# Performance work log

Measured on AMD Instinct MI355X. Metric: run time of the kernel, lower is better.

## Reference

```python
import jax, jax.numpy as jnp
import numpy as np

DEMO_T = 4
N_HEADS = 4
N_LAYERS = 2
EPS = 1e-5
IN_DIM = 512
FF_DIM = 128
TEMP = float(np.sqrt(IN_DIM))  # temperature=None -> sqrt(in_dim)


def setup_inputs() -> dict:
    key = jax.random.key(0)
    ks = jax.random.split(key, 12)
    B, d, T, H, W = 8, IN_DIM, 36, 7, 12
    s_in = 1.0 / np.sqrt(d)
    s_ff = 1.0 / np.sqrt(FF_DIM)
    f32 = jnp.float32
    return {
        "inputs": jax.random.normal(ks[0], (B, d, T, H, W), f32),
        "demo_wq": jax.random.normal(ks[1], (N_LAYERS, FF_DIM, d), f32) * s_in,
        "demo_wk": jax.random.normal(ks[2], (N_LAYERS, FF_DIM, d), f32) * s_in,
        "demo_wv": jax.random.normal(ks[3], (N_LAYERS, FF_DIM, d), f32) * s_in,
        "demo_wo": jax.random.normal(ks[4], (N_LAYERS, d, FF_DIM), f32) * s_ff,
        "obs_wq": jax.random.normal(ks[5], (N_LAYERS, FF_DIM, d), f32) * s_in,
        "obs_wk": jax.random.normal(ks[6], (N_LAYERS, FF_DIM, d), f32) * s_in,
        "obs_wv": jax.random.normal(ks[7], (N_LAYERS, FF_DIM, d), f32) * s_in,
        "obs_wo": jax.random.normal(ks[8], (N_LAYERS, d, FF_DIM), f32) * s_ff,
        "bn_gamma": jnp.ones((N_LAYERS, d), f32),
        "bn_beta": jnp.zeros((N_LAYERS, d), f32),
    }


def _conv1x1(w, x):
    # 1x1x1 Conv3d, bias=False == per-voxel channel mixing
    return jnp.einsum('od,bdthw->bothw', w, x)


def _forward(inputs, demo_wq, demo_wk, demo_wv, demo_wo,
             obs_wq, obs_wk, obs_wv, obs_wo, bn_gamma, bn_beta):
    B, d, T, H, W = inputs.shape
    HW = H * W
    obs_T = T - DEMO_T
    neg_inf = jnp.asarray(-jnp.inf, inputs.dtype)
    # causal log-mask over demo tokens, block-expanded to spatial positions
    tril = jnp.tril(jnp.ones((DEMO_T, DEMO_T), inputs.dtype))
    mask = jnp.repeat(jnp.repeat(tril, HW, axis=0), HW, axis=1)  # (dTHW, dTHW)
    log_mask = jnp.where(mask > 0, jnp.asarray(0.0, inputs.dtype), neg_inf)

    x = inputs
    for i in range(N_LAYERS):
        demo_in = x[:, :, :DEMO_T]   # [B,d,dT,H,W]
        obs_in = x[:, :, DEMO_T:]    # [B,d,oT,H,W]

        # --- demo self-attention (causal) ---
        def demo_heads(w):
            y = _conv1x1(w, demo_in)                      # [B,ff,dT,H,W]
            return y.reshape(B, N_HEADS, -1, DEMO_T * HW)  # [B,n,ch,dTHW]
        dq, dk, dv = demo_heads(demo_wq[i]), demo_heads(demo_wk[i]), demo_heads(demo_wv[i])
        dkq = jnp.einsum('bnci,bncj->bnij', dk, dq) / TEMP + log_mask
        dattn = jax.nn.softmax(dkq, axis=-1)               # softmax over j (as in source)
        dv_att = jnp.einsum('bncj,bnij->bnci', dv, dattn)  # attended demo values
        # NOTE: the source computes demo_out via demo_Outs + relu-skip but never
        # uses it downstream (dead code); only dv_att/dk feed the obs fusion.

        # --- obs attention, fused with demo keys/attended-values ---
        def obs_heads(w):
            y = _conv1x1(w, obs_in)                        # [B,ff,oT,H,W]
            y = y.reshape(B, N_HEADS, -1, obs_T, HW)
            return jnp.transpose(y, (0, 3, 1, 2, 4))       # [B,oT,n,ch,HW]
        oq, ok, ov = obs_heads(obs_wq[i]), obs_heads(obs_wk[i]), obs_heads(obs_wv[i])
        rep_k = jnp.broadcast_to(dk[:, None], (B, obs_T) + dk.shape[1:])
        rep_v = jnp.broadcast_to(dv_att[:, None], (B, obs_T) + dv_att.shape[1:])
        cat_k = jnp.concatenate([rep_k, ok], axis=-1)      # [B,oT,n,ch,(1+dT)HW]
        cat_v = jnp.concatenate([rep_v, ov], axis=-1)
        okq = jnp.einsum('btnci,btncj->btnij', cat_k, oq) / TEMP  # i=cat len, j=HW
        oattn = jax.nn.softmax(okq, axis=-1)               # softmax over j (source: dim=4)
        ov_att = jnp.einsum('btncj,btnji->btnci', cat_v, oattn)  # [B,oT,n,ch,HW]
        obs_out = _conv1x1(obs_wo[i],
                           jnp.transpose(ov_att, (0, 2, 3, 1, 4)).reshape(B, -1, obs_T, H, W))
        # skip (out_dim == in_dim), dropout=0 -> identity
        obs_res = obs_in + jax.nn.relu(obs_out)

        # shared BatchNorm3d (training-mode batch stats) over concatenated streams
        x = jnp.concatenate([demo_in, obs_res], axis=2)
        mean = x.mean(axis=(0, 2, 3, 4)).reshape(1, -1, 1, 1, 1)
        var = x.var(axis=(0, 2, 3, 4)).reshape(1, -1, 1, 1, 1)
        g = bn_gamma[i].reshape(1, -1, 1, 1, 1)
        b = bn_beta[i].reshape(1, -1, 1, 1, 1)
        x = g * (x - mean) * jax.lax.rsqrt(var + EPS) + b
    return x  # == out_dict['last']


def reference(inputs, demo_wq, demo_wk, demo_wv, demo_wo,
              obs_wq, obs_wk, obs_wv, obs_wo, bn_gamma, bn_beta):
    return _forward(inputs, demo_wq, demo_wk, demo_wv, demo_wo,
                    obs_wq, obs_wk, obs_wv, obs_wo, bn_gamma, bn_beta)
```

## Files before the change

### kernel.cpp

```cpp
#include <hip/hip_runtime.h>

#define B_N 8
#define D_N 512
#define T_N 36
#define HW_N 84
#define THW_N 3024
#define DT_N 4
#define OT_N 32
#define NH_N 4
#define FF_N 128
#define CH_N 32
#define DI_N 336
#define OI_N 2688
#define CAT_N 420
#define INV_TEMP 0.04419417382415922f
#define BN_EPS 1e-5f
#define INV_CNT (1.0f / 24192.0f)

#define SW_DWQ 0
#define SW_DWK 131072
#define SW_DWV 262144
#define SW_OWQ 393216
#define SW_OWK 524288
#define SW_OWV 655360
#define SW_OWO 786432
#define S_DQ   917504
#define S_DK   1261568
#define S_DV   1605632
#define S_DVA  1949696
#define S_OQ   2293760
#define S_OK   5046272
#define S_OV   7798784
#define S_OVA  10551296
#define S_XBF  13303808

typedef short bf16x8 __attribute__((ext_vector_type(8)));
typedef float f32x4 __attribute__((ext_vector_type(4)));

__device__ __forceinline__ short f2bf(float f) {
    unsigned u = __float_as_uint(f);
    u += 0x7fffu + ((u >> 16) & 1u);
    return (short)(u >> 16);
}
__device__ __forceinline__ float bf2f(short s) {
    return __uint_as_float(((unsigned)(unsigned short)s) << 16);
}

__global__ __launch_bounds__(256) void cvt_w_kernel(
    const float* __restrict__ s0, const float* __restrict__ s1,
    const float* __restrict__ s2, const float* __restrict__ s3,
    const float* __restrict__ s4, const float* __restrict__ s5,
    const float* __restrict__ s6, short* __restrict__ dst,
    float* __restrict__ stats)
{
    const int bid = blockIdx.x;
    if (bid == 0) {
        #pragma unroll
        for (int k = 0; k < 8; ++k) stats[threadIdx.x * 8 + k] = 0.f;
    }
    const int a = bid >> 6, blk = bid & 63;
    const float* src;
    switch (a) {
        case 0: src = s0; break; case 1: src = s1; break;
        case 2: src = s2; break; case 3: src = s3; break;
        case 4: src = s4; break; case 5: src = s5; break;
        default: src = s6;
    }
    const int idx = (blk * 256 + (int)threadIdx.x) * 8;
    float4 f0 = *reinterpret_cast<const float4*>(src + idx);
    float4 f1 = *reinterpret_cast<const float4*>(src + idx + 4);
    bf16x8 pk;
    pk[0] = f2bf(f0.x); pk[1] = f2bf(f0.y); pk[2] = f2bf(f0.z); pk[3] = f2bf(f0.w);
    pk[4] = f2bf(f1.x); pk[5] = f2bf(f1.y); pk[6] = f2bf(f1.z); pk[7] = f2bf(f1.w);
    *reinterpret_cast<bf16x8*>(dst + (size_t)a * 131072 + idx) = pk;
}

__global__ __launch_bounds__(256) void xin_kernel(
    const float* __restrict__ in_f, short* __restrict__ xbf,
    float* __restrict__ stats0)
{
    __shared__ short tile[48][65];
    __shared__ float red_s[16][64];
    __shared__ float red_q[16][64];

    const int bid = blockIdx.x;
    const int b = bid / 504, rem = bid % 504, tt = rem >> 3, cblk = rem & 7;
    const int t0 = tt * 48, c0 = cblk * 64;
    const int tid = threadIdx.x;
    const bool is_demo = (tt < 7);

    #pragma unroll
    for (int l0 = 0; l0 < 768; l0 += 256) {
        int l = l0 + tid;
        int cc = l / 12, tg = l % 12;
        size_t addr = ((size_t)b * D_N + c0 + cc) * THW_N + t0 + tg * 4;
        float4 v = *reinterpret_cast<const float4*>(in_f + addr);
        tile[tg * 4 + 0][cc] = f2bf(v.x);
        tile[tg * 4 + 1][cc] = f2bf(v.y);
        tile[tg * 4 + 2][cc] = f2bf(v.z);
        tile[tg * 4 + 3][cc] = f2bf(v.w);
    }
    __syncthreads();
    float psum[4] = {}, psq[4] = {};
    const int cg = tid & 15;
    #pragma unroll
    for (int l0 = 0; l0 < 768; l0 += 256) {
        int l = l0 + tid;
        int tk = l >> 4;
        short4 s4;
        s4.x = tile[tk][cg * 4 + 0];
        s4.y = tile[tk][cg * 4 + 1];
        s4.z = tile[tk][cg * 4 + 2];
        s4.w = tile[tk][cg * 4 + 3];
        *reinterpret_cast<short4*>(
            xbf + ((size_t)b * THW_N + t0 + tk) * 512 + c0 + cg * 4) = s4;
        if (is_demo) {
            float v0 = bf2f(s4.x), v1 = bf2f(s4.y), v2 = bf2f(s4.z), v3 = bf2f(s4.w);
            psum[0] += v0; psum[1] += v1; psum[2] += v2; psum[3] += v3;
            psq[0] += v0 * v0; psq[1] += v1 * v1; psq[2] += v2 * v2; psq[3] += v3 * v3;
        }
    }
    if (!is_demo) return;
    __syncthreads();
    #pragma unroll
    for (int j = 0; j < 4; ++j) {
        red_s[tid >> 4][cg * 4 + j] = psum[j];
        red_q[tid >> 4][cg * 4 + j] = psq[j];
    }
    __syncthreads();
    if (tid < 64) {
        float s = 0.f, q = 0.f;
        #pragma unroll
        for (int r = 0; r < 16; ++r) { s += red_s[r][tid]; q += red_q[r][tid]; }
        atomicAdd(&stats0[c0 + tid], s);
        atomicAdd(&stats0[512 + c0 + tid], q);
    }
}

__global__ __launch_bounds__(256) void proj_mfma_kernel(
    const short* __restrict__ xbf, short* __restrict__ ws, int layer)
{
    __shared__ short As[3][4096];
    __shared__ short Bs[1536];

    const int bid = blockIdx.x;
    const int b = bid / 63, ct = bid - b * 63;
    const bool is_demo = (ct < 7);
    const int woff = layer * 65536;
    const short* W0 = ws + (is_demo ? SW_DWQ : SW_OWQ) + woff;
    const short* W1 = ws + (is_demo ? SW_DWK : SW_OWK) + woff;
    const short* W2 = ws + (is_demo ? SW_DWV : SW_OWV) + woff;
    const int Ltok = is_demo ? DI_N : OI_N;
    const int colL = is_demo ? ct * 48 : (ct - 7) * 48;
    short* Yq = ws + (is_demo ? S_DQ : S_OQ);
    short* Yk = ws + (is_demo ? S_DK : S_OK);
    short* Yv = ws + (is_demo ? S_DV : S_OV);
    const short* Xb = xbf + ((size_t)b * THW_N + (is_demo ? 0 : DI_N) + colL) * 512;

    const int tid = threadIdx.x;
    const int lane = tid & 63, wv = tid >> 6;
    const int l15 = lane & 15, q = lane >> 4;

    f32x4 acc[3][2][3] = {};

    for (int k0 = 0; k0 < D_N; k0 += 32) {
        __syncthreads();
        const short* Wt[3] = {W0, W1, W2};
        #pragma unroll
        for (int wt = 0; wt < 3; ++wt) {
            #pragma unroll
            for (int h = 0; h < 2; ++h) {
                int c = tid + h * 256;
                int kc = c & 3, m = c >> 2;
                bf16x8 pk = *reinterpret_cast<const bf16x8*>(
                    Wt[wt] + (size_t)m * D_N + k0 + kc * 8);
                *reinterpret_cast<bf16x8*>(&As[wt][(kc * 128 + m) * 8]) = pk;
            }
        }
        if (tid < 192) {
            int n = tid % 48, kc = tid / 48;
            bf16x8 pk = *reinterpret_cast<const bf16x8*>(
                Xb + (size_t)n * 512 + k0 + kc * 8);
            *reinterpret_cast<bf16x8*>(&Bs[(kc * 48 + n) * 8]) = pk;
        }
        __syncthreads();

        bf16x8 bfr[3];
        #pragma unroll
        for (int nt = 0; nt < 3; ++nt)
            bfr[nt] = *reinterpret_cast<const bf16x8*>(&Bs[(q * 48 + nt * 16 + l15) * 8]);
        #pragma unroll
        for (int wt = 0; wt < 3; ++wt) {
            #pragma unroll
            for (int mt2 = 0; mt2 < 2; ++mt2) {
                bf16x8 afr = *reinterpret_cast<const bf16x8*>(
                    &As[wt][(q * 128 + wv * 32 + mt2 * 16 + l15) * 8]);
                #pragma unroll
                for (int nt = 0; nt < 3; ++nt)
                    acc[wt][mt2][nt] = __builtin_amdgcn_mfma_f32_16x16x32_bf16(
                        afr, bfr[nt], acc[wt][mt2][nt], 0, 0, 0);
            }
        }
    }

    #pragma unroll
    for (int mt2 = 0; mt2 < 2; ++mt2) {
        int mrow = wv * 32 + mt2 * 16 + q * 4;
        #pragma unroll
        for (int nt = 0; nt < 3; ++nt) {
            int token = colL + nt * 16 + l15;
            f32x4 aq = acc[0][mt2][nt] * INV_TEMP;
            short4 s4;
            s4.x = f2bf(aq[0]); s4.y = f2bf(aq[1]); s4.z = f2bf(aq[2]); s4.w = f2bf(aq[3]);
            *reinterpret_cast<short4*>(Yq + ((size_t)b * Ltok + token) * 128 + mrow) = s4;
            f32x4 ak = acc[1][mt2][nt];
            s4.x = f2bf(ak[0]); s4.y = f2bf(ak[1]); s4.z = f2bf(ak[2]); s4.w = f2bf(ak[3]);
            *reinterpret_cast<short4*>(Yk + ((size_t)b * Ltok + token) * 128 + mrow) = s4;
            #pragma unroll
            for (int r = 0; r < 4; ++r)
                Yv[((size_t)b * FF_N + mrow + r) * Ltok + token] = f2bf(acc[2][mt2][nt][r]);
        }
    }
}

template<int NT>
__device__ __forceinline__ void demo_core(
    const short* __restrict__ dqS, const short* __restrict__ dkS,
    const short* __restrict__ dvS, short* __restrict__ dvaS,
    short* __restrict__ Pt, int b, int n, int ti, int ih)
{
    constexpr int NTP = (NT + 1) & ~1;
    const int tid = threadIdx.x;
    const int lane = tid & 63, w = tid >> 6;
    const int l15 = lane & 15, q = lane >> 4;
    const int jmax = (ti + 1) * 84;

    const int irow = ih * 48 + w * 16 + l15;
    const int tokA = ti * 84 + (irow < 84 ? irow : 83);
    bf16x8 afr = *reinterpret_cast<const bf16x8*>(
        dkS + ((size_t)b * DI_N + tokA) * 128 + n * 32 + q * 8);

    f32x4 s[NT];
    #pragma unroll
    for (int nt = 0; nt < NT; ++nt) {
        bf16x8 bfr = *reinterpret_cast<const bf16x8*>(
            dqS + ((size_t)b * DI_N + nt * 16 + l15) * 128 + n * 32 + q * 8);
        f32x4 z = {};
        s[nt] = __builtin_amdgcn_mfma_f32_16x16x32_bf16(afr, bfr, z, 0, 0, 0);
    }

    const int mstart = jmax - (NT - 1) * 16;
    #pragma unroll
    for (int r = 0; r < 4; ++r) {
        if (l15 >= mstart) s[NT - 1][r] = -3.0e38f;
        float mx = s[0][r];
        #pragma unroll
        for (int nt = 1; nt < NT; ++nt) mx = fmaxf(mx, s[nt][r]);
        #pragma unroll
        for (int o = 1; o < 16; o <<= 1) mx = fmaxf(mx, __shfl_xor(mx, o));
        float sm = 0.f;
        #pragma unroll
        for (int nt = 0; nt < NT; ++nt) {
            float e = __expf(s[nt][r] - mx);
            s[nt][r] = e; sm += e;
        }
        #pragma unroll
        for (int o = 1; o < 16; o <<= 1) sm += __shfl_xor(sm, o);
        float inv = 1.f / sm;
        #pragma unroll
        for (int nt = 0; nt < NT; ++nt) s[nt][r] *= inv;
    }

    #pragma unroll
    for (int nt = 0; nt < NT; ++nt)
        #pragma unroll
        for (int r = 0; r < 4; ++r)
            Pt[(w * 16 + q * 4 + r) * 360 + nt * 16 + l15] = f2bf(s[nt][r]);
    if (NTP != NT) {
        #pragma unroll
        for (int r = 0; r < 4; ++r)
            Pt[(w * 16 + q * 4 + r) * 360 + NT * 16 + l15] = 0;
    }
    __syncthreads();

    f32x4 oacc[2] = {};
    #pragma unroll
    for (int kk = 0; kk < NTP / 2; ++kk) {
        bf16x8 pb = *reinterpret_cast<const bf16x8*>(
            &Pt[(w * 16 + l15) * 360 + kk * 32 + q * 8]);
        #pragma unroll
        for (int ct = 0; ct < 2; ++ct) {
            bf16x8 va = *reinterpret_cast<const bf16x8*>(
                dvS + ((size_t)b * FF_N + n * 32 + ct * 16 + l15) * DI_N + kk * 32 + q * 8);
            oacc[ct] = __builtin_amdgcn_mfma_f32_16x16x32_bf16(va, pb, oacc[ct], 0, 0, 0);
        }
    }

    const int ig = ih * 48 + w * 16 + l15;
    if (ig < 84) {
        #pragma unroll
        for (int ct = 0; ct < 2; ++ct)
            #pragma unroll
            for (int r = 0; r < 4; ++r)
                dvaS[((size_t)b * FF_N + n * 32 + ct * 16 + q * 4 + r) * DI_N + ti * 84 + ig] =
                    f2bf(oacc[ct][r]);
    }
}

__global__ __launch_bounds__(192) void demo_attn_mfma_kernel(const short* __restrict__ ws)
{
    __shared__ short Pt[48 * 360];

    const short* dqS = ws + S_DQ;
    const short* dkS = ws + S_DK;
    const short* dvS = ws + S_DV;
    short* dvaS = const_cast<short*>(ws) + S_DVA;

    const int bid = blockIdx.x;
    const int ih = bid & 1, ti = (bid >> 1) & 3;
    const int n = (bid >> 3) & 3, b = bid >> 5;

    switch (ti) {
        case 0: demo_core<6>(dqS, dkS, dvS, dvaS, Pt, b, n, ti, ih); break;
        case 1: demo_core<11>(dqS, dkS, dvS, dvaS, Pt, b, n, ti, ih); break;
        case 2: demo_core<16>(dqS, dkS, dvS, dvaS, Pt, b, n, ti, ih); break;
        default: demo_core<21>(dqS, dkS, dvS, dvaS, Pt, b, n, ti, ih); break;
    }
}

__global__ __launch_bounds__(256, 4) void obs_attn_mfma_kernel(const short* __restrict__ ws)
{
    __shared__ short Qt[96 * 40];
    __shared__ short Kt[64 * 40];
    __shared__ short Vs[32 * 72];
    __shared__ short Pt[96 * 72];

    const short* dkS = ws + S_DK;
    const short* dvaS = ws + S_DVA;
    const short* oqS = ws + S_OQ;
    const short* okS = ws + S_OK;
    const short* ovS = ws + S_OV;
    short* ovaS = const_cast<short*>(ws) + S_OVA;

    const int bid = blockIdx.x;
    const int b = bid >> 7, rem = bid & 127, t = rem >> 2, n = rem & 3;

    const int tid = threadIdx.x;
    const int lane = tid & 63, wv = tid >> 6;
    const int l15 = lane & 15, q = lane >> 4;

    for (int l = tid; l < 384; l += 256) {
        int i = l >> 2, c0 = (l & 3) * 8;
        bf16x8 pk = {0,0,0,0,0,0,0,0};
        if (i < HW_N)
            pk = *reinterpret_cast<const bf16x8*>(
                oqS + ((size_t)b * OI_N + t * 84 + i) * 128 + n * 32 + c0);
        *reinterpret_cast<bf16x8*>(&Qt[i * 40 + c0]) = pk;
    }

    const int pv_mt = wv & 1;
    const int pv_nb = wv >> 1;
    f32x4 oacc[3] = {};

    for (int jc = 0; jc < 448; jc += 64) {
        __syncthreads();
        {
            int jl = tid >> 2, c0 = (tid & 3) * 8;
            int jg = jc + jl;
            bf16x8 pk = {0,0,0,0,0,0,0,0};
            if (jg < DI_N)
                pk = *reinterpret_cast<const bf16x8*>(
                    dkS + ((size_t)b * DI_N + jg) * 128 + n * 32 + c0);
            else if (jg < CAT_N)
                pk = *reinterpret_cast<const bf16x8*>(
                    okS + ((size_t)b * OI_N + t * 84 + (jg - DI_N)) * 128 + n * 32 + c0);
            *reinterpret_cast<bf16x8*>(&Kt[jl * 40 + c0]) = pk;
        }
        {
            int c = tid >> 3, j0 = (tid & 7) * 8;
            int jg0 = jc + j0;
            const short* dvaRow = dvaS + ((size_t)b * FF_N + n * 32 + c) * DI_N;
            const short* ovRow = ovS + ((size_t)b * FF_N + n * 32 + c) * OI_N + t * 84;
            bf16x8 pk;
            if (jg0 + 8 <= DI_N) {
                pk = *reinterpret_cast<const bf16x8*>(dvaRow + jg0);
            } else if (jg0 >= DI_N && jg0 + 8 <= CAT_N) {
                short4 lo = *reinterpret_cast<const short4*>(ovRow + (jg0 - DI_N));
                short4 hi = *reinterpret_cast<const short4*>(ovRow + (jg0 - DI_N) + 4);
                pk[0]=lo.x; pk[1]=lo.y; pk[2]=lo.z; pk[3]=lo.w;
                pk[4]=hi.x; pk[5]=hi.y; pk[6]=hi.z; pk[7]=hi.w;
            } else {
                #pragma unroll
                for (int p = 0; p < 8; ++p) {
                    int jg = jg0 + p;
                    pk[p] = (jg < DI_N) ? dvaRow[jg]
                          : ((jg < CAT_N) ? ovRow[jg - DI_N] : (short)0);
                }
            }
            *reinterpret_cast<bf16x8*>(&Vs[c * 72 + j0]) = pk;
        }
        __syncthreads();

        f32x4 s[6];
        bf16x8 afr = *reinterpret_cast<const bf16x8*>(&Kt[(wv * 16 + l15) * 40 + q * 8]);
        #pragma unroll
        for (int nt = 0; nt < 6; ++nt) {
            bf16x8 bfr = *reinterpret_cast<const bf16x8*>(&Qt[(nt * 16 + l15) * 40 + q * 8]);
            f32x4 z = {};
            s[nt] = __builtin_amdgcn_mfma_f32_16x16x32_bf16(afr, bfr, z, 0, 0, 0);
        }
        float inv[4];
        #pragma unroll
        for (int r = 0; r < 4; ++r) {
            if (l15 >= 4) s[5][r] = -3.0e38f;
            float m2 = s[0][r];
            #pragma unroll
            for (int nt2 = 1; nt2 < 6; ++nt2) m2 = fmaxf(m2, s[nt2][r]);
            #pragma unroll
            for (int o = 1; o < 16; o <<= 1) m2 = fmaxf(m2, __shfl_xor(m2, o));
            float sm = 0.f;
            #pragma unroll
            for (int nt2 = 0; nt2 < 6; ++nt2) { float e = __expf(s[nt2][r] - m2); s[nt2][r] = e; sm += e; }
            #pragma unroll
            for (int o = 1; o < 16; o <<= 1) sm += __shfl_xor(sm, o);
            inv[r] = 1.f / sm;
        }
        #pragma unroll
        for (int nt = 0; nt < 6; ++nt) {
            short4 pk4;
            pk4.x = f2bf(s[nt][0] * inv[0]);
            pk4.y = f2bf(s[nt][1] * inv[1]);
            pk4.z = f2bf(s[nt][2] * inv[2]);
            pk4.w = f2bf(s[nt][3] * inv[3]);
            *reinterpret_cast<short4*>(&Pt[(nt * 16 + l15) * 72 + wv * 16 + q * 4]) = pk4;
        }
        __syncthreads();

        #pragma unroll
        for (int kk = 0; kk < 2; ++kk) {
            bf16x8 va = *reinterpret_cast<const bf16x8*>(&Vs[(pv_mt * 16 + l15) * 72 + kk * 32 + q * 8]);
            #pragma unroll
            for (int u = 0; u < 3; ++u) {
                int nt = pv_nb + u * 2;
                bf16x8 pb = *reinterpret_cast<const bf16x8*>(&Pt[(nt * 16 + l15) * 72 + kk * 32 + q * 8]);
                oacc[u] = __builtin_amdgcn_mfma_f32_16x16x32_bf16(va, pb, oacc[u], 0, 0, 0);
            }
        }
    }

    #pragma unroll
    for (int u = 0; u < 3; ++u) {
        int i = (pv_nb + u * 2) * 16 + l15;
        if (i < HW_N) {
            short4 st;
            st.x = f2bf(oacc[u][0]); st.y = f2bf(oacc[u][1]);
            st.z = f2bf(oacc[u][2]); st.w = f2bf(oacc[u][3]);
            *reinterpret_cast<short4*>(
                ovaS + (((size_t)b * OT_N + t) * 84 + i) * 128 + n * 32 + pv_mt * 16 + q * 4) = st;
        }
    }
}

__global__ __launch_bounds__(256) void outproj_mfma_kernel(
    short* __restrict__ xbf, const short* __restrict__ ws, int layer,
    float* __restrict__ stats)
{
    __shared__ float redS[4][32];
    __shared__ float redQ[4][32];

    const int bid = blockIdx.x;
    const int t8 = bid & 7;
    const int rr = bid >> 3;
    const int c32 = rr & 15;
    const int tc = rr >> 4;
    const int tchunk = tc * 8 + t8;
    const int o0 = c32 * 32;

    const int tid = threadIdx.x;
    const int lane = tid & 63, wv = tid >> 6;
    const int l15 = lane & 15, q = lane >> 4;

    const int g0 = tchunk * 192 + wv * 48;
    const int b = g0 / OI_N;
    const size_t xbase = (size_t)(g0 + DI_N * (b + 1)) * 512 + o0;

    const short* Wo = ws + SW_OWO + layer * 65536;
    const short* ova = ws + S_OVA;

    bf16x8 afr[2][4];
    #pragma unroll
    for (int mt = 0; mt < 2; ++mt)
        #pragma unroll
        for (int kc = 0; kc < 4; ++kc)
            afr[mt][kc] = *reinterpret_cast<const bf16x8*>(
                Wo + (size_t)(o0 + mt * 16 + l15) * FF_N + kc * 32 + q * 8);

    float csum[2][4] = {}, csq[2][4] = {};

    #pragma unroll
    for (int nt = 0; nt < 3; ++nt) {
        const int g = g0 + nt * 16;
        const short* ovaT = ova + (size_t)(g + l15) * FF_N + q * 8;
        bf16x8 bfr[4];
        #pragma unroll
        for (int kc = 0; kc < 4; ++kc)
            bfr[kc] = *reinterpret_cast<const bf16x8*>(ovaT + kc * 32);

        f32x4 acc[2] = {};
        #pragma unroll
        for (int kc = 0; kc < 4; ++kc) {
            acc[0] = __builtin_amdgcn_mfma_f32_16x16x32_bf16(afr[0][kc], bfr[kc], acc[0], 0, 0, 0);
            acc[1] = __builtin_amdgcn_mfma_f32_16x16x32_bf16(afr[1][kc], bfr[kc], acc[1], 0, 0, 0);
        }

        #pragma unroll
        for (int mt = 0; mt < 2; ++mt) {
            short* p = xbf + xbase + (size_t)(nt * 16 + l15) * 512 + mt * 16 + q * 4;
            short4 old4 = *reinterpret_cast<short4*>(p);
            float ov[4] = {bf2f(old4.x), bf2f(old4.y), bf2f(old4.z), bf2f(old4.w)};
            short4 nw;
            short* nwp = &nw.x;
            #pragma unroll
            for (int r = 0; r < 4; ++r) {
                float v = acc[mt][r];
                float y = ov[r] + (v > 0.f ? v : 0.f);
                short ybf = f2bf(y);
                nwp[r] = ybf;
                float yr = bf2f(ybf);
                csum[mt][r] += yr;
                csq[mt][r] += yr * yr;
            }
            *reinterpret_cast<short4*>(p) = nw;
        }
    }

    #pragma unroll
    for (int mt = 0; mt < 2; ++mt) {
        #pragma unroll
        for (int r = 0; r < 4; ++r) {
            float s = csum[mt][r], qq = csq[mt][r];
            #pragma unroll
            for (int o = 1; o < 16; o <<= 1) {
                s += __shfl_xor(s, o);
                qq += __shfl_xor(qq, o);
            }
            if (l15 == 0) {
                redS[wv][mt * 16 + q * 4 + r] = s;
                redQ[wv][mt * 16 + q * 4 + r] = qq;
            }
        }
    }
    __syncthreads();
    if (tid < 32) {
        float s = redS[0][tid] + redS[1][tid] + redS[2][tid] + redS[3][tid];
        float qq = redQ[0][tid] + redQ[1][tid] + redQ[2][tid] + redQ[3][tid];
        atomicAdd(&stats[o0 + tid], s);
        atomicAdd(&stats[512 + o0 + tid], qq);
    }
}

__global__ __launch_bounds__(256) void bn_mid_kernel(
    short* __restrict__ xbf, const float* __restrict__ stats,
    const float* __restrict__ gamma, const float* __restrict__ beta,
    float* __restrict__ stats_next)
{
    __shared__ float red_s[4][512];
    __shared__ float red_q[4][512];

    const int bid = blockIdx.x;
    const int b = bid / 63, tt = bid % 63;
    const int t0 = tt * 48;
    const bool is_demo = (tt < 7);
    const int tid = threadIdx.x;
    const int chg = tid & 63;
    const int trow = tid >> 6;

    float mean[8], rs[8], g[8], bb[8];
    #pragma unroll
    for (int j = 0; j < 8; ++j) {
        int c = chg * 8 + j;
        float m = stats[c] * INV_CNT;
        float var = stats[512 + c] * INV_CNT - m * m;
        mean[j] = m;
        rs[j] = rsqrtf(var + BN_EPS);
        g[j] = gamma[c];
        bb[j] = beta[c];
    }

    float psum[8] = {}, psq[8] = {};
    #pragma unroll
    for (int it = 0; it < 12; ++it) {
        int tok = t0 + it * 4 + trow;
        short* p = xbf + ((size_t)b * THW_N + tok) * 512 + chg * 8;
        bf16x8 v = *reinterpret_cast<bf16x8*>(p);
        bf16x8 w;
        #pragma unroll
        for (int j = 0; j < 8; ++j) {
            float y = g[j] * (bf2f(v[j]) - mean[j]) * rs[j] + bb[j];
            short yb = f2bf(y);
            w[j] = yb;
            if (is_demo) {
                float yr = bf2f(yb);
                psum[j] += yr; psq[j] += yr * yr;
            }
        }
        *reinterpret_cast<bf16x8*>(p) = w;
    }
    if (!is_demo) return;
    #pragma unroll
    for (int j = 0; j < 8; ++j) {
        red_s[trow][chg * 8 + j] = psum[j];
        red_q[trow][chg * 8 + j] = psq[j];
    }
    __syncthreads();
    #pragma unroll
    for (int h = 0; h < 2; ++h) {
        int c = tid + h * 256;
        float s = red_s[0][c] + red_s[1][c] + red_s[2][c] + red_s[3][c];
        float qq = red_q[0][c] + red_q[1][c] + red_q[2][c] + red_q[3][c];
        atomicAdd(&stats_next[c], s);
        atomicAdd(&stats_next[512 + c], qq);
    }
}

__global__ __launch_bounds__(256) void bn_out_kernel(
    const short* __restrict__ xbf, float* __restrict__ out_f,
    const float* __restrict__ stats,
    const float* __restrict__ gamma, const float* __restrict__ beta)
{
    __shared__ float tile[48][65];

    const int bid = blockIdx.x;
    const int b = bid / 504, rem = bid % 504, tt = rem >> 3, cblk = rem & 7;
    const int t0 = tt * 48, c0 = cblk * 64;
    const int tid = threadIdx.x;
    const int cg = tid & 15;

    float mean[4], rs[4], g[4], bb[4];
    #pragma unroll
    for (int j = 0; j < 4; ++j) {
        int c = c0 + cg * 4 + j;
        float m = stats[c] * INV_CNT;
        float var = stats[512 + c] * INV_CNT - m * m;
        mean[j] = m; rs[j] = rsqrtf(var + BN_EPS);
        g[j] = gamma[c]; bb[j] = beta[c];
    }

    #pragma unroll
    for (int l0 = 0; l0 < 768; l0 += 256) {
        int l = l0 + tid;
        int tok = l >> 4;
        short4 v = *reinterpret_cast<const short4*>(
            xbf + ((size_t)b * THW_N + t0 + tok) * 512 + c0 + cg * 4);
        tile[tok][cg * 4 + 0] = g[0] * (bf2f(v.x) - mean[0]) * rs[0] + bb[0];
        tile[tok][cg * 4 + 1] = g[1] * (bf2f(v.y) - mean[1]) * rs[1] + bb[1];
        tile[tok][cg * 4 + 2] = g[2] * (bf2f(v.z) - mean[2]) * rs[2] + bb[2];
        tile[tok][cg * 4 + 3] = g[3] * (bf2f(v.w) - mean[3]) * rs[3] + bb[3];
    }
    __syncthreads();
    #pragma unroll
    for (int l0 = 0; l0 < 768; l0 += 256) {
        int l = l0 + tid;
        int cc = l / 12, tg = l % 12;
        float4 o;
        o.x = tile[tg * 4 + 0][cc];
        o.y = tile[tg * 4 + 1][cc];
        o.z = tile[tg * 4 + 2][cc];
        o.w = tile[tg * 4 + 3][cc];
        *reinterpret_cast<float4*>(
            out_f + ((size_t)b * D_N + c0 + cc) * THW_N + t0 + tg * 4) = o;
    }
}

extern "C" void kernel_launch(void* const* d_in, const int* in_sizes, int n_in,
                              void* d_out, int out_size, void* d_ws, size_t ws_size,
                              hipStream_t stream)
{
    const float* inp  = (const float*)d_in[0];
    const float* dwq  = (const float*)d_in[1];
    const float* dwk  = (const float*)d_in[2];
    const float* dwv  = (const float*)d_in[3];
    const float* owq  = (const float*)d_in[5];
    const float* owk  = (const float*)d_in[6];
    const float* owv  = (const float*)d_in[7];
    const float* owo  = (const float*)d_in[8];
    const float* gam  = (const float*)d_in[9];
    const float* bet  = (const float*)d_in[10];
    float* x  = (float*)d_out;
    float* stats = (float*)d_ws;
    short* wsS = (short*)(stats + 2048);
    short* xbf = wsS + S_XBF;

    cvt_w_kernel<<<448, 256, 0, stream>>>(dwq, dwk, dwv, owq, owk, owv, owo, wsS, stats);
    xin_kernel<<<4032, 256, 0, stream>>>(inp, xbf, stats);

    for (int layer = 0; layer < 2; ++layer) {
        float* stL = stats + layer * 1024;
        size_t coff = (size_t)layer * D_N;
        proj_mfma_kernel<<<504, 256, 0, stream>>>(xbf, wsS, layer);
        demo_attn_mfma_kernel<<<256, 192, 0, stream>>>(wsS);
        obs_attn_mfma_kernel<<<1024, 256, 0, stream>>>(wsS);
        outproj_mfma_kernel<<<1792, 256, 0, stream>>>(xbf, wsS, layer, stL);
        if (layer == 0) {
            bn_mid_kernel<<<504, 256, 0, stream>>>(
                xbf, stL, gam + coff, bet + coff, stats + 1024);
        } else {
            bn_out_kernel<<<4032, 256, 0, stream>>>(
                xbf, x, stL, gam + coff, bet + coff);
        }
    }
    (void)in_sizes; (void)n_in; (void)out_size; (void)ws_size;
}
```

Baseline: 321.6 us.

## Restructure QKV projection to per-wave 16-token tiles reading weights from global

The QKV projection kernel drops its shared-memory staging. Each wave now owns a 16-token tile, keeps the full 512-wide input fragment in registers, and streams all three 128x512 weight matrices straight from global/L2 into MFMA. This removes the __syncthreads barriers and LDS traffic and raises the wave count. In exchange, every wave rereads the whole weight set from cache, and register pressure rises a lot (16 bf16x8 input fragments plus 24 accumulators) under launch_bounds(256,2).

After: 455.4 us. +41.6%, slower.

```diff
diff --git a/kernel.cpp b/kernel.cpp
--- a/kernel.cpp
+++ b/kernel.cpp
@@ -137,89 +137,65 @@
     }
 }
 
-__global__ __launch_bounds__(256) void proj_mfma_kernel(
+__global__ __launch_bounds__(256, 2) void proj_mfma_kernel(
     const short* __restrict__ xbf, short* __restrict__ ws, int layer)
 {
-    __shared__ short As[3][4096];
-    __shared__ short Bs[1536];
-
-    const int bid = blockIdx.x;
-    const int b = bid / 63, ct = bid - b * 63;
-    const bool is_demo = (ct < 7);
+    const int tid = threadIdx.x;
+    const int lane = tid & 63, wv = tid >> 6;
+    const int l15 = lane & 15, q = lane >> 4;
+
+    const int gid = blockIdx.x * 4 + wv;
+    const int b = gid / 189;
+    const int r = gid - b * 189;
+    const bool is_demo = (r < 21);
     const int woff = layer * 65536;
     const short* W0 = ws + (is_demo ? SW_DWQ : SW_OWQ) + woff;
     const short* W1 = ws + (is_demo ? SW_DWK : SW_OWK) + woff;
     const short* W2 = ws + (is_demo ? SW_DWV : SW_OWV) + woff;
     const int Ltok = is_demo ? DI_N : OI_N;
-    const int colL = is_demo ? ct * 48 : (ct - 7) * 48;
+    const int tok0 = is_demo ? r * 16 : (r - 21) * 16;
     short* Yq = ws + (is_demo ? S_DQ : S_OQ);
     short* Yk = ws + (is_demo ? S_DK : S_OK);
     short* Yv = ws + (is_demo ? S_DV : S_OV);
-    const short* Xb = xbf + ((size_t)b * THW_N + (is_demo ? 0 : DI_N) + colL) * 512;
-
-    const int tid = threadIdx.x;
-    const int lane = tid & 63, wv = tid >> 6;
-    const int l15 = lane & 15, q = lane >> 4;
-
-    f32x4 acc[3][2][3] = {};
-
-    for (int k0 = 0; k0 < D_N; k0 += 32) {
-        __syncthreads();
-        const short* Wt[3] = {W0, W1, W2};
+    const short* Xb = xbf + ((size_t)b * THW_N + (is_demo ? 0 : DI_N) + tok0) * 512;
+
+    bf16x8 bfr[16];
+    #pragma unroll
+    for (int kc = 0; kc < 16; ++kc)
+        bfr[kc] = *reinterpret_cast<const bf16x8*>(
+            Xb + (size_t)l15 * 512 + kc * 32 + q * 8);
+
+    f32x4 acc[3][8] = {};
+    const short* Wt[3] = {W0, W1, W2};
+
+    #pragma unroll
+    for (int kc = 0; kc < 16; ++kc) {
         #pragma unroll
         for (int wt = 0; wt < 3; ++wt) {
             #pragma unroll
-            for (int h = 0; h < 2; ++h) {
-                int c = tid + h * 256;
-                int kc = c & 3, m = c >> 2;
-                bf16x8 pk = *reinterpret_cast<const bf16x8*>(
-                    Wt[wt] + (size_t)m * D_N + k0 + kc * 8);
-                *reinterpret_cast<bf16x8*>(&As[wt][(kc * 128 + m) * 8]) = pk;
+            for (int mt = 0; mt < 8; ++mt) {
+                bf16x8 afr = *reinterpret_cast<const bf16x8*>(
+                    Wt[wt] + (size_t)(mt * 16 + l15) * 512 + kc * 32 + q * 8);
+                acc[wt][mt] = __builtin_amdgcn_mfma_f32_16x16x32_bf16(
+                    afr, bfr[kc], acc[wt][mt], 0, 0, 0);
             }
         }
-        if (tid < 192) {
-            int n = tid % 48, kc = tid / 48;
-            bf16x8 pk = *reinterpret_cast<const bf16x8*>(
-                Xb + (size_t)n * 512 + k0 + kc * 8);
-            *reinterpret_cast<bf16x8*>(&Bs[(kc * 48 + n) * 8]) = pk;
-        }
-        __syncthreads();
-
-        bf16x8 bfr[3];
-        #pragma unroll
-        for (int nt = 0; nt < 3; ++nt)
-            bfr[nt] = *reinterpret_cast<const bf16x8*>(&Bs[(q * 48 + nt * 16 + l15) * 8]);
-        #pragma unroll
-        for (int wt = 0; wt < 3; ++wt) {
-            #pragma unroll
-            for (int mt2 = 0; mt2 < 2; ++mt2) {
-                bf16x8 afr = *reinterpret_cast<const bf16x8*>(
-                    &As[wt][(q * 128 + wv * 32 + mt2 * 16 + l15) * 8]);
-                #pragma unroll
-                for (int nt = 0; nt < 3; ++nt)
-                    acc[wt][mt2][nt] = __builtin_amdgcn_mfma_f32_16x16x32_bf16(
-                        afr, bfr[nt], acc[wt][mt2][nt], 0, 0, 0);
-            }
-        }
-    }
-
-    #pragma unroll
-    for (int mt2 = 0; mt2 < 2; ++mt2) {
-        int mrow = wv * 32 + mt2 * 16 + q * 4;
-        #pragma unroll
-        for (int nt = 0; nt < 3; ++nt) {
-            int token = colL + nt * 16 + l15;
-            f32x4 aq = acc[0][mt2][nt] * INV_TEMP;
-            short4 s4;
-            s4.x = f2bf(aq[0]); s4.y = f2bf(aq[1]); s4.z = f2bf(aq[2]); s4.w = f2bf(aq[3]);
-            *reinterpret_cast<short4*>(Yq + ((size_t)b * Ltok + token) * 128 + mrow) = s4;
-            f32x4 ak = acc[1][mt2][nt];
-            s4.x = f2bf(ak[0]); s4.y = f2bf(ak[1]); s4.z = f2bf(ak[2]); s4.w = f2bf(ak[3]);
-            *reinterpret_cast<short4*>(Yk + ((size_t)b * Ltok + token) * 128 + mrow) = s4;
-            #pragma unroll
-            for (int r = 0; r < 4; ++r)
-                Yv[((size_t)b * FF_N + mrow + r) * Ltok + token] = f2bf(acc[2][mt2][nt][r]);
-        }
+    }
+
+    const int token = tok0 + l15;
+    #pragma unroll
+    for (int mt = 0; mt < 8; ++mt) {
+        const int mrow = mt * 16 + q * 4;
+        f32x4 aq = acc[0][mt] * INV_TEMP;
+        short4 s4;
+        s4.x = f2bf(aq[0]); s4.y = f2bf(aq[1]); s4.z = f2bf(aq[2]); s4.w = f2bf(aq[3]);
+        *reinterpret_cast<short4*>(Yq + ((size_t)b * Ltok + token) * 128 + mrow) = s4;
+        f32x4 ak = acc[1][mt];
+        s4.x = f2bf(ak[0]); s4.y = f2bf(ak[1]); s4.z = f2bf(ak[2]); s4.w = f2bf(ak[3]);
+        *reinterpret_cast<short4*>(Yk + ((size_t)b * Ltok + token) * 128 + mrow) = s4;
+        #pragma unroll
+        for (int rr = 0; rr < 4; ++rr)
+            Yv[((size_t)b * FF_N + mrow + rr) * Ltok + token] = f2bf(acc[2][mt][rr]);
     }
 }
 
@@ -697,7 +673,7 @@
     for (int layer = 0; layer < 2; ++layer) {
         float* stL = stats + layer * 1024;
         size_t coff = (size_t)layer * D_N;
-        proj_mfma_kernel<<<504, 256, 0, stream>>>(xbf, wsS, layer);
+        proj_mfma_kernel<<<378, 256, 0, stream>>>(xbf, wsS, layer);
         demo_attn_mfma_kernel<<<256, 192, 0, stream>>>(wsS);
         obs_attn_mfma_kernel<<<1024, 256, 0, stream>>>(wsS);
         outproj_mfma_kernel<<<1792, 256, 0, stream>>>(xbf, wsS, layer, stL);
```

## Split QKV projection over output halves and load tiles via global_load_lds

Applied to the files above, without the earlier changes.

The QKV projection kernel now splits the 128 output channels across two blocks, doubling the grid to 1008 blocks. Each block handles a 64-row slice of the three weight matrices. Tiles are copied straight from global memory into LDS with the global_load_lds builtin instead of going through registers, and the K step grows from 32 to 64, halving the number of barrier pairs. The goal is more parallelism, lower register pressure and cheaper tile staging, at the cost of loading the activation tile twice (once per half).

After: 341.9 us. 6.3% more time.

```diff
diff --git a/kernel.cpp b/kernel.cpp
--- a/kernel.cpp
+++ b/kernel.cpp
@@ -36,6 +36,11 @@
 
 typedef short bf16x8 __attribute__((ext_vector_type(8)));
 typedef float f32x4 __attribute__((ext_vector_type(4)));
+typedef unsigned int u32;
+
+#define GLD16(SRC, DST) __builtin_amdgcn_global_load_lds( \
+    (const __attribute__((address_space(1))) u32*)(SRC), \
+    (__attribute__((address_space(3))) u32*)(DST), 16, 0, 0)
 
 __device__ __forceinline__ short f2bf(float f) {
     unsigned u = __float_as_uint(f);
@@ -141,10 +146,16 @@
     const short* __restrict__ xbf, short* __restrict__ ws, int layer)
 {
     __shared__ short As[3][4096];
-    __shared__ short Bs[1536];
+    __shared__ short Bs[3072];
+
+    const int tid = threadIdx.x;
+    const int lane = tid & 63, wv = tid >> 6;
+    const int l15 = lane & 15, q = lane >> 4;
 
     const int bid = blockIdx.x;
-    const int b = bid / 63, ct = bid - b * 63;
+    const int mh = bid & 1;
+    const int rem = bid >> 1;
+    const int b = rem / 63, ct = rem - b * 63;
     const bool is_demo = (ct < 7);
     const int woff = layer * 65536;
     const short* W0 = ws + (is_demo ? SW_DWQ : SW_OWQ) + woff;
@@ -157,69 +168,68 @@
     short* Yv = ws + (is_demo ? S_DV : S_OV);
     const short* Xb = xbf + ((size_t)b * THW_N + (is_demo ? 0 : DI_N) + colL) * 512;
 
-    const int tid = threadIdx.x;
-    const int lane = tid & 63, wv = tid >> 6;
-    const int l15 = lane & 15, q = lane >> 4;
-
-    f32x4 acc[3][2][3] = {};
-
-    for (int k0 = 0; k0 < D_N; k0 += 32) {
+    const short* rp[3];
+    rp[0] = W0 + (size_t)(mh * 64 + lane) * 512;
+    rp[1] = W1 + (size_t)(mh * 64 + lane) * 512;
+    rp[2] = W2 + (size_t)(mh * 64 + lane) * 512;
+    const short* bp[2];
+    #pragma unroll
+    for (int h = 0; h < 2; ++h) {
+        int c = h * 192 + wv * 64 + lane;
+        bp[h] = Xb + (size_t)(c % 48) * 512 + (c / 48) * 8;
+    }
+
+    f32x4 acc[3][3] = {};
+
+    for (int k0 = 0; k0 < D_N; k0 += 64) {
         __syncthreads();
-        const short* Wt[3] = {W0, W1, W2};
-        #pragma unroll
-        for (int wt = 0; wt < 3; ++wt) {
-            #pragma unroll
-            for (int h = 0; h < 2; ++h) {
-                int c = tid + h * 256;
-                int kc = c & 3, m = c >> 2;
-                bf16x8 pk = *reinterpret_cast<const bf16x8*>(
-                    Wt[wt] + (size_t)m * D_N + k0 + kc * 8);
-                *reinterpret_cast<bf16x8*>(&As[wt][(kc * 128 + m) * 8]) = pk;
-            }
-        }
-        if (tid < 192) {
-            int n = tid % 48, kc = tid / 48;
-            bf16x8 pk = *reinterpret_cast<const bf16x8*>(
-                Xb + (size_t)n * 512 + k0 + kc * 8);
-            *reinterpret_cast<bf16x8*>(&Bs[(kc * 48 + n) * 8]) = pk;
+        #pragma unroll
+        for (int h = 0; h < 2; ++h) {
+            #pragma unroll
+            for (int wt = 0; wt < 3; ++wt)
+                GLD16(rp[wt] + k0 + (h * 4 + wv) * 8,
+                      &As[wt][(h * 256 + wv * 64) * 8]);
+        }
+        if (wv < 3) {
+            GLD16(bp[0] + k0, &Bs[(wv * 64) * 8]);
+            GLD16(bp[1] + k0, &Bs[(192 + wv * 64) * 8]);
         }
         __syncthreads();
 
-        bf16x8 bfr[3];
-        #pragma unroll
-        for (int nt = 0; nt < 3; ++nt)
-            bfr[nt] = *reinterpret_cast<const bf16x8*>(&Bs[(q * 48 + nt * 16 + l15) * 8]);
-        #pragma unroll
-        for (int wt = 0; wt < 3; ++wt) {
-            #pragma unroll
-            for (int mt2 = 0; mt2 < 2; ++mt2) {
+        #pragma unroll
+        for (int kk = 0; kk < 2; ++kk) {
+            const int kc = kk * 4 + q;
+            bf16x8 bfr[3];
+            #pragma unroll
+            for (int nt = 0; nt < 3; ++nt)
+                bfr[nt] = *reinterpret_cast<const bf16x8*>(
+                    &Bs[(kc * 48 + nt * 16 + l15) * 8]);
+            #pragma unroll
+            for (int wt = 0; wt < 3; ++wt) {
                 bf16x8 afr = *reinterpret_cast<const bf16x8*>(
-                    &As[wt][(q * 128 + wv * 32 + mt2 * 16 + l15) * 8]);
+                    &As[wt][(kc * 64 + wv * 16 + l15) * 8]);
                 #pragma unroll
                 for (int nt = 0; nt < 3; ++nt)
-                    acc[wt][mt2][nt] = __builtin_amdgcn_mfma_f32_16x16x32_bf16(
-                        afr, bfr[nt], acc[wt][mt2][nt], 0, 0, 0);
+                    acc[wt][nt] = __builtin_amdgcn_mfma_f32_16x16x32_bf16(
+                        afr, bfr[nt], acc[wt][nt], 0, 0, 0);
             }
         }
     }
 
-    #pragma unroll
-    for (int mt2 = 0; mt2 < 2; ++mt2) {
-        int mrow = wv * 32 + mt2 * 16 + q * 4;
-        #pragma unroll
-        for (int nt = 0; nt < 3; ++nt) {
-            int token = colL + nt * 16 + l15;
-            f32x4 aq = acc[0][mt2][nt] * INV_TEMP;
-            short4 s4;
-            s4.x = f2bf(aq[0]); s4.y = f2bf(aq[1]); s4.z = f2bf(aq[2]); s4.w = f2bf(aq[3]);
-            *reinterpret_cast<short4*>(Yq + ((size_t)b * Ltok + token) * 128 + mrow) = s4;
-            f32x4 ak = acc[1][mt2][nt];
-            s4.x = f2bf(ak[0]); s4.y = f2bf(ak[1]); s4.z = f2bf(ak[2]); s4.w = f2bf(ak[3]);
-            *reinterpret_cast<short4*>(Yk + ((size_t)b * Ltok + token) * 128 + mrow) = s4;
-            #pragma unroll
-            for (int r = 0; r < 4; ++r)
-                Yv[((size_t)b * FF_N + mrow + r) * Ltok + token] = f2bf(acc[2][mt2][nt][r]);
-        }
+    const int mrow = mh * 64 + wv * 16 + q * 4;
+    #pragma unroll
+    for (int nt = 0; nt < 3; ++nt) {
+        const int token = colL + nt * 16 + l15;
+        f32x4 aq = acc[0][nt] * INV_TEMP;
+        short4 s4;
+        s4.x = f2bf(aq[0]); s4.y = f2bf(aq[1]); s4.z = f2bf(aq[2]); s4.w = f2bf(aq[3]);
+        *reinterpret_cast<short4*>(Yq + ((size_t)b * Ltok + token) * 128 + mrow) = s4;
+        f32x4 ak = acc[1][nt];
+        s4.x = f2bf(ak[0]); s4.y = f2bf(ak[1]); s4.z = f2bf(ak[2]); s4.w = f2bf(ak[3]);
+        *reinterpret_cast<short4*>(Yk + ((size_t)b * Ltok + token) * 128 + mrow) = s4;
+        #pragma unroll
+        for (int rr = 0; rr < 4; ++rr)
+            Yv[((size_t)b * FF_N + mrow + rr) * Ltok + token] = f2bf(acc[2][nt][rr]);
     }
 }
 
@@ -697,7 +707,7 @@
     for (int layer = 0; layer < 2; ++layer) {
         float* stL = stats + layer * 1024;
         size_t coff = (size_t)layer * D_N;
-        proj_mfma_kernel<<<504, 256, 0, stream>>>(xbf, wsS, layer);
+        proj_mfma_kernel<<<1008, 256, 0, stream>>>(xbf, wsS, layer);
         demo_attn_mfma_kernel<<<256, 192, 0, stream>>>(wsS);
         obs_attn_mfma_kernel<<<1024, 256, 0, stream>>>(wsS);
         outproj_mfma_kernel<<<1792, 256, 0, stream>>>(xbf, wsS, layer, stL);
```
